# Kernel tuning notes

Measured on AMD Instinct MI355X. Metric: run time of the kernel, lower is better.

The kernel has to match this reference:

```python
import jax, jax.numpy as jnp
import numpy as np

LBDA = 0.1  # softmin temperature used by OTAM_cum_dist in this repo family


def otam_cum_dist(dists):
    # dists: [Q, S, Tq, Ts] frame-to-frame distances
    Q, S, Tq, Ts = dists.shape
    d = jnp.pad(dists, ((0, 0), (0, 0), (0, 0), (1, 1)))  # zero-pad support axis -> width W = Ts + 2
    W = Ts + 2
    # top row: cum[0, m] = d[0, m] + cum[0, m-1]  (plain cumulative sum, cum[0,0]=0 since d[...,0]=0)
    row0 = jnp.cumsum(d[:, :, 0, :], axis=-1)  # [Q, S, W]

    # column m gets the extra term prev_row[m] only at the first (m=1) and last (m=W-1) columns
    incl = jnp.zeros(W - 1, dtype=bool).at[0].set(True).at[-1].set(True)

    def row_step(prev_row, d_row):
        # prev_row, d_row: [Q, S, W]; move column axis to front for the scan
        d_cols = jnp.moveaxis(d_row[:, :, 1:], -1, 0)        # d[l, m],    m = 1..W-1  -> [W-1, Q, S]
        prev_mm1 = jnp.moveaxis(prev_row[:, :, :-1], -1, 0)  # prev[m-1]
        prev_m = jnp.moveaxis(prev_row[:, :, 1:], -1, 0)     # prev[m]

        def col_step(carry, xs):
            # carry = cum[l, m-1] (starts at cum[l,0] = 0)
            d_m, p_mm1, p_m, inc = xs
            t3 = jnp.where(inc, -p_m / LBDA, -jnp.inf)
            neg = jnp.stack([-p_mm1 / LBDA, -carry / LBDA, t3])  # [3, Q, S]
            val = d_m - LBDA * jax.nn.logsumexp(neg, axis=0)     # softmin recurrence
            return val, val

        _, cols = jax.lax.scan(col_step, jnp.zeros((Q, S), d.dtype),
                               (d_cols, prev_mm1, prev_m, incl))
        new_row = jnp.concatenate([jnp.zeros((Q, S, 1), d.dtype),
                                   jnp.moveaxis(cols, 0, -1)], axis=-1)
        return new_row, None

    d_rows = jnp.moveaxis(d[:, :, 1:, :], 2, 0)  # [Tq-1, Q, S, W]
    last_row, _ = jax.lax.scan(row_step, row0, d_rows)
    return last_row[:, :, -1]  # cum_dists[..., -1, -1] -> [Q, S]


def setup_inputs() -> dict:
    key = jax.random.key(0)
    similarity = jax.random.uniform(key, (2048, 128, 16, 16), dtype=jnp.float32)
    return {"similarity": similarity}


def reference(similarity):
    distance = 1.0 - similarity
    votes = otam_cum_dist(distance) + otam_cum_dist(jnp.swapaxes(distance, -1, -2))
    return -(0.5 * votes)  # [query count, support count]
```

## Files before the change

### kernel.cpp

```cpp
#include <hip/hip_runtime.h>


#define K2   14.4269504088896340736f
#define LL2  0.069314718055994530942f

__device__ __forceinline__ float softmin2(float a, float b) {
    float mn = fminf(a, b);
    float t  = __builtin_amdgcn_exp2f(-K2 * fabsf(a - b));
    return mn - LL2 * __builtin_amdgcn_logf(1.0f + t);
}

__device__ __forceinline__ float softmin3(float a, float b, float c) {
    float mn = fminf(fminf(a, b), c);
    float s = __builtin_amdgcn_exp2f(-K2 * (a - mn))
            + __builtin_amdgcn_exp2f(-K2 * (b - mn))
            + __builtin_amdgcn_exp2f(-K2 * (c - mn));
    return mn - LL2 * __builtin_amdgcn_logf(s);
}

__device__ __forceinline__ void dp_row(float* R, const float* dr) {
    float diag = R[0];
    float oldR = R[1];
    R[1] = dr[0] + softmin3(diag, R[0], oldR);
    diag = oldR;
#pragma unroll
    for (int m = 2; m <= 16; ++m) {
        float o = R[m];
        R[m] = dr[m - 1] + softmin2(diag, R[m - 1]);
        diag = o;
    }
    R[17] = softmin3(diag, R[16], R[17]);
}

__device__ __forceinline__ void dp_col(float* C, const float* dr) {
    float diag2 = C[0];
    C[0] = C[0] + dr[0];
#pragma unroll
    for (int l = 1; l < 16; ++l) {
        float o = C[l];
        C[l] = dr[l] + softmin2(diag2, o);
        diag2 = o;
    }
}

__global__ __launch_bounds__(256, 2)
void otam_fused_kernel(const float* __restrict__ sim, float* __restrict__ out) {
    const int t  = threadIdx.x & 63;
    const int wv = threadIdx.x >> 6;
    const int pair0 = blockIdx.x * 256 + wv * 64;

    __shared__ float lds_all[4 * 2048];
    float* lds = lds_all + (wv << 11);

    const int u = t >> 3;
    const int c = t & 7;

    const float* gbase = sim + (((size_t)(pair0 + u)) << 8) + (c << 2);
    float* wbase = lds + ((u * 8 + (c ^ u)) << 2);

    float R[18], C[16], dr[16];
    float4 ld[8];

#define LOADN(cc)                                                                  \
    _Pragma("unroll")                                                              \
    for (int i = 0; i < 8; ++i)                                                    \
        ld[i] = *reinterpret_cast<const float4*>(gbase + i * 2048 + (cc) * 32);

#define WRITEC()                                                                   \
    _Pragma("unroll")                                                              \
    for (int i = 0; i < 8; ++i) {                                                  \
        float4 w;                                                                  \
        w.x = 1.0f - ld[i].x; w.y = 1.0f - ld[i].y;                                \
        w.z = 1.0f - ld[i].z; w.w = 1.0f - ld[i].w;                                \
        *reinterpret_cast<float4*>(wbase + i * 256) = w;                           \
    }

#define READR(rr)                                                                  \
    _Pragma("unroll")                                                              \
    for (int k = 0; k < 4; ++k) {                                                  \
        float4 v = *reinterpret_cast<const float4*>(                               \
            lds + t * 32 + ((((rr) * 4 + k) ^ c) << 2));                           \
        dr[k * 4 + 0] = v.x; dr[k * 4 + 1] = v.y;                                  \
        dr[k * 4 + 2] = v.z; dr[k * 4 + 3] = v.w;                                  \
    }

    LOADN(0);
    WRITEC();

    READR(0);
    R[0] = 0.0f;
#pragma unroll
    for (int m = 1; m <= 16; ++m) R[m] = R[m - 1] + dr[m - 1];
    R[17] = R[16];
    C[0] = dr[0];
#pragma unroll
    for (int l = 1; l < 16; ++l)
        C[l] = dr[l] + softmin3(0.0f, 0.0f, C[l - 1]);

    LOADN(1);

    READR(1);
    dp_row(R, dr);
    dp_col(C, dr);

    for (int cc = 1; cc < 8; ++cc) {
        WRITEC();
        READR(0);
        dp_row(R, dr);
        dp_col(C, dr);
        if (cc < 7) LOADN(cc + 1);
        READR(1);
        dp_row(R, dr);
        dp_col(C, dr);
    }

    {
        float diag2 = C[0];
#pragma unroll
        for (int l = 1; l < 16; ++l) {
            float o = C[l];
            C[l] = softmin3(diag2, o, C[l - 1]);
            diag2 = o;
        }
    }

    out[pair0 + t] = -0.5f * (R[17] + C[15]);
#undef LOADN
#undef WRITEC
#undef READR
}

extern "C" void kernel_launch(void* const* d_in, const int* in_sizes, int n_in,
                              void* d_out, int out_size, void* d_ws, size_t ws_size,
                              hipStream_t stream) {
    const float* sim = (const float*)d_in[0];
    float* out = (float*)d_out;
    int npairs = in_sizes[0] >> 8;
    int grid = npairs >> 8;
    otam_fused_kernel<<<grid, 256, 0, stream>>>(sim, out);
}
```

Measured before the change: 53.36 us.

## Double-buffer global loads with two register sets and shrink blocks to two waves

Each wave now stages two 32-column chunks into a doubled LDS buffer per step. Two register buffers (A, B) keep two global loads in flight while four DP rows run, where before only one load overlapped two rows. Blocks drop to 128 threads with launch bounds of 3 per CU, and LDS per wave doubles to 16 KB. The deeper prefetch is meant to hide memory latency better, at the cost of more registers and LDS, which may reduce occupancy.

```diff
diff --git a/kernel.cpp b/kernel.cpp
--- a/kernel.cpp
+++ b/kernel.cpp
@@ -43,14 +43,14 @@
     }
 }
 
-__global__ __launch_bounds__(256, 2)
+__global__ __launch_bounds__(128, 3)
 void otam_fused_kernel(const float* __restrict__ sim, float* __restrict__ out) {
     const int t  = threadIdx.x & 63;
     const int wv = threadIdx.x >> 6;
-    const int pair0 = blockIdx.x * 256 + wv * 64;
+    const int pair0 = blockIdx.x * 128 + wv * 64;
 
-    __shared__ float lds_all[4 * 2048];
-    float* lds = lds_all + (wv << 11);
+    __shared__ float lds_all[2 * 4096];
+    float* lds = lds_all + (wv << 12);
 
     const int u = t >> 3;
     const int c = t & 7;
@@ -59,33 +59,37 @@
     float* wbase = lds + ((u * 8 + (c ^ u)) << 2);
 
     float R[18], C[16], dr[16];
-    float4 ld[8];
+    float4 A[8], B[8];
 
-#define LOADN(cc)                                                                  \
+#define LOADG(buf, cc)                                                             \
     _Pragma("unroll")                                                              \
     for (int i = 0; i < 8; ++i)                                                    \
-        ld[i] = *reinterpret_cast<const float4*>(gbase + i * 2048 + (cc) * 32);
+        buf[i] = *reinterpret_cast<const float4*>(gbase + i * 2048 + (cc) * 32);
 
-#define WRITEC()                                                                   \
+#define WRITEG(buf, slot)                                                          \
     _Pragma("unroll")                                                              \
     for (int i = 0; i < 8; ++i) {                                                  \
         float4 w;                                                                  \
-        w.x = 1.0f - ld[i].x; w.y = 1.0f - ld[i].y;                                \
-        w.z = 1.0f - ld[i].z; w.w = 1.0f - ld[i].w;                                \
-        *reinterpret_cast<float4*>(wbase + i * 256) = w;                           \
+        w.x = 1.0f - buf[i].x; w.y = 1.0f - buf[i].y;                              \
+        w.z = 1.0f - buf[i].z; w.w = 1.0f - buf[i].w;                              \
+        *reinterpret_cast<float4*>(wbase + (slot) * 2048 + i * 256) = w;           \
     }
 
 #define READR(rr)                                                                  \
     _Pragma("unroll")                                                              \
     for (int k = 0; k < 4; ++k) {                                                  \
         float4 v = *reinterpret_cast<const float4*>(                               \
-            lds + t * 32 + ((((rr) * 4 + k) ^ c) << 2));                           \
+            lds + ((rr) >> 1) * 2048 + t * 32 + (((((rr) & 1) * 4 + k) ^ c) << 2)); \
         dr[k * 4 + 0] = v.x; dr[k * 4 + 1] = v.y;                                  \
         dr[k * 4 + 2] = v.z; dr[k * 4 + 3] = v.w;                                  \
     }
 
-    LOADN(0);
-    WRITEC();
+    LOADG(A, 0);
+    LOADG(B, 1);
+    WRITEG(A, 0);
+    LOADG(A, 2);
+    WRITEG(B, 1);
+    LOADG(B, 3);
 
     READR(0);
     R[0] = 0.0f;
@@ -97,21 +101,19 @@
     for (int l = 1; l < 16; ++l)
         C[l] = dr[l] + softmin3(0.0f, 0.0f, C[l - 1]);
 
-    LOADN(1);
+    READR(1); dp_row(R, dr); dp_col(C, dr);
+    READR(2); dp_row(R, dr); dp_col(C, dr);
+    READR(3); dp_row(R, dr); dp_col(C, dr);
 
-    READR(1);
-    dp_row(R, dr);
-    dp_col(C, dr);
-
-    for (int cc = 1; cc < 8; ++cc) {
-        WRITEC();
-        READR(0);
-        dp_row(R, dr);
-        dp_col(C, dr);
-        if (cc < 7) LOADN(cc + 1);
-        READR(1);
-        dp_row(R, dr);
-        dp_col(C, dr);
+    for (int s = 1; s < 4; ++s) {
+        WRITEG(A, 0);
+        if (s < 3) LOADG(A, 2 * s + 2);
+        WRITEG(B, 1);
+        if (s < 3) LOADG(B, 2 * s + 3);
+        READR(0); dp_row(R, dr); dp_col(C, dr);
+        READR(1); dp_row(R, dr); dp_col(C, dr);
+        READR(2); dp_row(R, dr); dp_col(C, dr);
+        READR(3); dp_row(R, dr); dp_col(C, dr);
     }
 
     {
@@ -125,8 +127,8 @@
     }
 
     out[pair0 + t] = -0.5f * (R[17] + C[15]);
-#undef LOADN
-#undef WRITEC
+#undef LOADG
+#undef WRITEG
 #undef READR
 }
 
@@ -136,6 +138,6 @@
     const float* sim = (const float*)d_in[0];
     float* out = (float*)d_out;
     int npairs = in_sizes[0] >> 8;
-    int grid = npairs >> 8;
-    otam_fused_kernel<<<grid, 256, 0, stream>>>(sim, out);
+    int grid = npairs >> 7;
+    otam_fused_kernel<<<grid, 128, 0, stream>>>(sim, out);
 }
```

Result: slower. 71.33 us (+33.7%).
